# Kernel optimization log

Measured on AMD Instinct MI355X. Metric: run time of the kernel, lower is better.

Reference implementation:

```python
import jax, jax.numpy as jnp
import numpy as np

N = 320   # coalition size (number of prefix steps)
D = 512   # input_dim / attention weight_dim


def setup_inputs() -> dict:
    key = jax.random.key(0)
    ks = jax.random.split(key, 10)
    s = 1.0 / np.sqrt(D)  # torch Linear default init range
    u = lambda k, shape: jax.random.uniform(k, shape, jnp.float32, -s, s)
    return {
        "x": jax.random.normal(ks[0], (N, D), jnp.float32),
        "goal": jax.random.normal(ks[1], (D,), jnp.float32),
        "Wq": u(ks[2], (D, D)), "bq": u(ks[3], (D,)),
        "Wk": u(ks[4], (D, D)), "bk": u(ks[5], (D,)),
        "Wv": u(ks[6], (D, D)), "bv": u(ks[7], (D,)),
        # norm_col_init(std=0.1): small column-normalized weights; bias zero-filled
        "Wc": 0.01 * jax.random.normal(ks[8], (1, 2 * D), jnp.float32),
        "bc": jnp.zeros((1,), jnp.float32),
    }


def reference(x, goal, Wq, bq, Wk, bk, Wv, bv, Wc, bc):
    # x: [n, d] coalition features. goal is unused by the original forward.
    n, d = x.shape
    q = x @ Wq.T + bq  # [n, d]
    k = x @ Wk.T + bk
    v = x @ Wv.T + bv
    scores = (q @ k.T) / jnp.sqrt(jnp.asarray(d, x.dtype))  # [n, n]

    # Prefix lengths j = 1..n-1. For each j, attention over coalition[:j]:
    # softmax over keys < j (rows < j are the only valid queries), then the
    # AttentionLayer global feature = mean over query rows of attn @ v.
    j = jnp.arange(1, n)                          # [n-1]
    idx = jnp.arange(n)
    prefix_mask = idx[None, :] < j[:, None]       # [n-1, n], True for k < j
    neg = jnp.finfo(scores.dtype).min
    masked = jnp.where(prefix_mask[:, None, :], scores[None, :, :], neg)  # [n-1, n, n]
    att = jax.nn.softmax(masked, axis=-1)         # rows >= j are garbage, masked below
    # mean over valid query rows i < j, fused before multiplying by V:
    pooled = jnp.sum(att * prefix_mask[:, :, None], axis=1) / j[:, None].astype(x.dtype)  # [n-1, n]
    feats = pooled @ v                            # [n-1, d] global feature per prefix

    # j = 0 uses a zero feature vector
    features = jnp.concatenate([jnp.zeros((1, d), x.dtype), feats], axis=0)  # [n, d]
    cat = jnp.concatenate([features, x], axis=1)  # [n, 2d]
    vals = cat @ Wc.T + bc                        # [n, 1] critic outputs
    return jnp.sum(vals)[None]                    # scalar value, shape [1]
```

## Files before the change

kernel.cpp:

```cpp
#include <hip/hip_runtime.h>

#define NC 320
#define DIM 512

__global__ __launch_bounds__(256) void gemm_qk_part(
    const float* __restrict__ x,
    const float* __restrict__ Wq, const float* __restrict__ Wk,
    float* __restrict__ part)
{
  const int z = blockIdx.z;
  const float* __restrict__ W = (z & 8) ? Wk : Wq;
  const int kb = (z & 7) * 64;
  const int i0 = blockIdx.y * 64;
  const int c0 = blockIdx.x * 64;

  __shared__ __align__(16) float As[32][68];
  __shared__ __align__(16) float Bs[32][68];

  const int t  = threadIdx.x;
  const int sr = t >> 2;
  const int kc = (t & 3) << 3;
  const int ty = t >> 4;
  const int tx = t & 15;

  float acc[4][4] = {};

  const float* xp = x + (i0 + sr) * DIM + kc;
  const float* wp = W + (c0 + sr) * DIM + kc;

  for (int k0 = kb; k0 < kb + 64; k0 += 32) {
    const float4 xa = *(const float4*)(xp + k0);
    const float4 xb = *(const float4*)(xp + k0 + 4);
    const float4 wa = *(const float4*)(wp + k0);
    const float4 wb = *(const float4*)(wp + k0 + 4);
    __syncthreads();
    As[kc+0][sr]=xa.x; As[kc+1][sr]=xa.y; As[kc+2][sr]=xa.z; As[kc+3][sr]=xa.w;
    As[kc+4][sr]=xb.x; As[kc+5][sr]=xb.y; As[kc+6][sr]=xb.z; As[kc+7][sr]=xb.w;
    Bs[kc+0][sr]=wa.x; Bs[kc+1][sr]=wa.y; Bs[kc+2][sr]=wa.z; Bs[kc+3][sr]=wa.w;
    Bs[kc+4][sr]=wb.x; Bs[kc+5][sr]=wb.y; Bs[kc+6][sr]=wb.z; Bs[kc+7][sr]=wb.w;
    __syncthreads();
    #pragma unroll
    for (int kk = 0; kk < 32; ++kk) {
      const float4 a4 = *(const float4*)&As[kk][ty * 4];
      const float4 b4 = *(const float4*)&Bs[kk][tx * 4];
      const float a[4] = {a4.x, a4.y, a4.z, a4.w};
      const float b[4] = {b4.x, b4.y, b4.z, b4.w};
      #pragma unroll
      for (int i = 0; i < 4; ++i)
        #pragma unroll
        for (int j = 0; j < 4; ++j)
          acc[i][j] = fmaf(a[i], b[j], acc[i][j]);
    }
  }

  float* outp = part + (size_t)z * NC * DIM;
  #pragma unroll
  for (int i = 0; i < 4; ++i) {
    float4 o = {acc[i][0], acc[i][1], acc[i][2], acc[i][3]};
    *(float4*)&outp[(i0 + ty*4 + i) * DIM + c0 + tx*4] = o;
  }
}

__global__ __launch_bounds__(256) void reduce_qk(
    const float* __restrict__ part,
    const float* __restrict__ bq, const float* __restrict__ bk,
    float* __restrict__ q, float* __restrict__ k)
{
  const int mat = blockIdx.y;
  const int f   = blockIdx.x * 256 + threadIdx.x;
  const int row = f >> 7;
  const int col = (f & 127) * 4;
  const float* bias = mat ? bk : bq;
  float4 s = *(const float4*)&bias[col];
  const size_t off = (size_t)row * DIM + col;
  #pragma unroll
  for (int sp = 0; sp < 8; ++sp) {
    const float4 p = *(const float4*)&part[(size_t)(mat*8+sp) * NC * DIM + off];
    s.x += p.x; s.y += p.y; s.z += p.z; s.w += p.w;
  }
  float* out = mat ? k : q;
  *(float4*)&out[off] = s;
}

__global__ __launch_bounds__(256) void scores_part(
    const float* __restrict__ q, const float* __restrict__ k,
    float* __restrict__ part)
{
  const int z  = blockIdx.z;
  const int kb = z * 64;
  const int i0 = blockIdx.y * 64;
  const int j0 = blockIdx.x * 64;

  __shared__ __align__(16) float As[32][68];
  __shared__ __align__(16) float Bs[32][68];

  const int t  = threadIdx.x;
  const int sr = t >> 2;
  const int kc = (t & 3) << 3;
  const int ty = t >> 4;
  const int tx = t & 15;

  float acc[4][4] = {};

  const float* qp = q + (i0 + sr) * DIM + kc;
  const float* kp = k + (j0 + sr) * DIM + kc;

  for (int k0 = kb; k0 < kb + 64; k0 += 32) {
    const float4 qa = *(const float4*)(qp + k0);
    const float4 qb = *(const float4*)(qp + k0 + 4);
    const float4 ka = *(const float4*)(kp + k0);
    const float4 kb4= *(const float4*)(kp + k0 + 4);
    __syncthreads();
    As[kc+0][sr]=qa.x; As[kc+1][sr]=qa.y; As[kc+2][sr]=qa.z; As[kc+3][sr]=qa.w;
    As[kc+4][sr]=qb.x; As[kc+5][sr]=qb.y; As[kc+6][sr]=qb.z; As[kc+7][sr]=qb.w;
    Bs[kc+0][sr]=ka.x; Bs[kc+1][sr]=ka.y; Bs[kc+2][sr]=ka.z; Bs[kc+3][sr]=ka.w;
    Bs[kc+4][sr]=kb4.x;Bs[kc+5][sr]=kb4.y;Bs[kc+6][sr]=kb4.z;Bs[kc+7][sr]=kb4.w;
    __syncthreads();
    #pragma unroll
    for (int kk = 0; kk < 32; ++kk) {
      const float4 a4 = *(const float4*)&As[kk][ty * 4];
      const float4 b4 = *(const float4*)&Bs[kk][tx * 4];
      const float a[4] = {a4.x, a4.y, a4.z, a4.w};
      const float b[4] = {b4.x, b4.y, b4.z, b4.w};
      #pragma unroll
      for (int i = 0; i < 4; ++i)
        #pragma unroll
        for (int j = 0; j < 4; ++j)
          acc[i][j] = fmaf(a[i], b[j], acc[i][j]);
    }
  }

  float* outp = part + (size_t)z * NC * NC;
  #pragma unroll
  for (int i = 0; i < 4; ++i) {
    float4 o = {acc[i][0], acc[i][1], acc[i][2], acc[i][3]};
    *(float4*)&outp[(i0 + ty*4 + i) * NC + j0 + tx*4] = o;
  }
}

__global__ __launch_bounds__(256) void reduce_S(
    const float* __restrict__ part, float* __restrict__ S)
{
  const int f = blockIdx.x * 256 + threadIdx.x;
  const size_t off = (size_t)f * 4;
  float4 s = {0.f, 0.f, 0.f, 0.f};
  #pragma unroll
  for (int sp = 0; sp < 8; ++sp) {
    const float4 p = *(const float4*)&part[(size_t)sp * NC * NC + off];
    s.x += p.x; s.y += p.y; s.z += p.z; s.w += p.w;
  }
  const float scale = 0.044194173824159216f;
  s.x *= scale; s.y *= scale; s.z *= scale; s.w *= scale;
  *(float4*)&S[off] = s;
}

__global__ __launch_bounds__(256) void compute_h(
    const float* __restrict__ Wv, const float* __restrict__ Wc,
    float* __restrict__ h)
{
  const int e  = blockIdx.x * 256 + threadIdx.x;
  const int d0 = blockIdx.y * 32;
  float s = 0.f;
  #pragma unroll
  for (int d = 0; d < 32; ++d)
    s = fmaf(Wv[(d0 + d) * DIM + e], Wc[d0 + d], s);
  atomicAdd(&h[e], s);
}

__global__ __launch_bounds__(256) void row_ops(
    const float* __restrict__ S, float* __restrict__ P)
{
  const int i    = blockIdx.x;
  const int t    = threadIdx.x;
  const int lane = t & 63;
  const int wave = t >> 6;

  __shared__ float e[NC];
  __shared__ float Warr[NC];
  __shared__ float Csuf[NC + 1];
  __shared__ float wred[4];

  for (int kk = t; kk < NC; kk += 256) e[kk] = S[i * NC + kk];
  __syncthreads();

  float m = -1e30f;
  for (int kk = t; kk < NC; kk += 256) m = fmaxf(m, e[kk]);
  #pragma unroll
  for (int off = 32; off; off >>= 1) m = fmaxf(m, __shfl_down(m, off));
  if (lane == 0) wred[wave] = m;
  __syncthreads();
  m = fmaxf(fmaxf(wred[0], wred[1]), fmaxf(wred[2], wred[3]));

  for (int kk = t; kk < NC; kk += 256) e[kk] = __expf(e[kk] - m);
  __syncthreads();

  if (wave == 0) {
    float carry = 0.f;
    #pragma unroll
    for (int c = 0; c < 5; ++c) {
      const int idx = c * 64 + lane;
      float val = e[idx];
      #pragma unroll
      for (int off = 1; off < 64; off <<= 1) {
        const float nv = __shfl_up(val, off);
        if (lane >= off) val += nv;
      }
      const float incl = val + carry;
      const int j = idx + 1;
      if (j < NC) Warr[j] = (j > i) ? 1.f / ((float)j * incl) : 0.f;
      carry += __shfl(val, 63);
    }
    if (lane == 0) Warr[0] = 0.f;

    carry = 0.f;
    #pragma unroll
    for (int c = 4; c >= 0; --c) {
      const int idx = c * 64 + lane;
      float val = Warr[idx];
      #pragma unroll
      for (int off = 1; off < 64; off <<= 1) {
        const float nv = __shfl_down(val, off);
        if (lane + off < 64) val += nv;
      }
      Csuf[idx] = val + carry;
      carry += __shfl(val, 0);
    }
    if (lane == 0) Csuf[NC] = 0.f;
  }
  __syncthreads();

  for (int kk = t; kk < NC; kk += 256) {
    const int mm = (i > kk) ? i : kk;
    atomicAdd(&P[kk], e[kk] * Csuf[mm + 1]);
  }
}

__global__ __launch_bounds__(256) void finalize(
    const float* __restrict__ x, const float* __restrict__ P,
    const float* __restrict__ h, const float* __restrict__ Wc,
    const float* __restrict__ bc, const float* __restrict__ bv,
    float* __restrict__ out)
{
  const int kk   = blockIdx.x;
  const int t    = threadIdx.x;
  const int lane = t & 63;
  const int wave = t >> 6;

  __shared__ float tmp[4];
  __shared__ float tmp2[8];

  const float pk = P[kk];
  const float* xr = x + kk * DIM;
  float s = 0.f;
  for (int e = t; e < DIM; e += 256)
    s += xr[e] * fmaf(pk, h[e], Wc[DIM + e]);
  #pragma unroll
  for (int off = 32; off; off >>= 1) s += __shfl_down(s, off);
  if (lane == 0) tmp[wave] = s;

  if (kk == 0) {
    float ec = 0.f, ep = 0.f;
    for (int d = t; d < DIM; d += 256) ec += bv[d] * Wc[d];
    for (int mIdx = t; mIdx < NC; mIdx += 256) ep += P[mIdx];
    #pragma unroll
    for (int off = 32; off; off >>= 1) {
      ec += __shfl_down(ec, off);
      ep += __shfl_down(ep, off);
    }
    if (lane == 0) { tmp2[wave] = ec; tmp2[4 + wave] = ep; }
  }
  __syncthreads();

  if (t == 0) {
    float tot = tmp[0] + tmp[1] + tmp[2] + tmp[3];
    atomicAdd(out, tot);
    if (kk == 0) {
      const float c  = tmp2[0] + tmp2[1] + tmp2[2] + tmp2[3];
      const float sp = tmp2[4] + tmp2[5] + tmp2[6] + tmp2[7];
      atomicAdd(out, c * sp + (float)NC * bc[0]);
    }
  }
}

extern "C" void kernel_launch(void* const* d_in, const int* in_sizes, int n_in,
                              void* d_out, int out_size, void* d_ws, size_t ws_size,
                              hipStream_t stream) {
  const float* x  = (const float*)d_in[0];
  const float* Wq = (const float*)d_in[2];
  const float* bq = (const float*)d_in[3];
  const float* Wk = (const float*)d_in[4];
  const float* bk = (const float*)d_in[5];
  const float* Wv = (const float*)d_in[6];
  const float* bv = (const float*)d_in[7];
  const float* Wc = (const float*)d_in[8];
  const float* bc = (const float*)d_in[9];

  float* ws     = (float*)d_ws;
  float* q      = ws;
  float* k      = q + NC * DIM;
  float* S      = k + NC * DIM;
  float* P      = S + NC * NC;
  float* h      = P + NC;
  float* partQK = h + DIM;
  float* partS  = partQK + 16 * NC * DIM;
  float* out = (float*)d_out;

  hipMemsetAsync(P, 0, (NC + DIM) * sizeof(float), stream);
  hipMemsetAsync(out, 0, sizeof(float), stream);

  gemm_qk_part<<<dim3(8, 5, 16), 256, 0, stream>>>(x, Wq, Wk, partQK);
  reduce_qk<<<dim3(160, 2), 256, 0, stream>>>(partQK, bq, bk, q, k);
  compute_h<<<dim3(2, 16), 256, 0, stream>>>(Wv, Wc, h);
  scores_part<<<dim3(5, 5, 8), 256, 0, stream>>>(q, k, partS);
  reduce_S<<<100, 256, 0, stream>>>(partS, S);
  row_ops<<<NC, 256, 0, stream>>>(S, P);
  finalize<<<NC, 256, 0, stream>>>(x, P, h, Wc, bc, bv, out);
}
```

Before: 120.2 us.

## Fuse split-K reductions into consumers and precompute per-row critic projections

Removes reduce_qk and reduce_S by having the scores GEMM sum the Q/K split-K partials (plus biases) while loading tiles, and having the row softmax kernel sum the score partials on load. Replaces compute_h and finalize with one kernel that computes h = Wv^T Wc_feat and per-row u = x·h + c, accumulating the x·Wc_x term directly. row_ops then dots P with u in-block instead of atomically building P, cutting launch count from 7 to 4. The trade-off is redundant partial-sum reads: each scores tile re-reads 8 partials per Q/K element across 5 tile columns, and the hu kernel runs a serial 512-step loop per thread on only 20 blocks.

```diff
diff --git a/kernel.cpp b/kernel.cpp
--- a/kernel.cpp
+++ b/kernel.cpp
@@ -61,30 +61,73 @@
   }
 }
 
-__global__ __launch_bounds__(256) void reduce_qk(
+__global__ __launch_bounds__(256) void hu(
+    const float* __restrict__ x,  const float* __restrict__ Wv,
+    const float* __restrict__ bv, const float* __restrict__ Wc,
+    const float* __restrict__ bc,
+    float* __restrict__ u, float* __restrict__ out)
+{
+  const int t    = threadIdx.x;
+  const int lane = t & 63;
+  const int wave = t >> 6;
+
+  __shared__ __align__(16) float hsh[DIM];
+  __shared__ __align__(16) float wxs[DIM];
+  __shared__ float wsum[4];
+
+  float s0 = 0.f, s1 = 0.f;
+  #pragma unroll 8
+  for (int d = 0; d < DIM; ++d) {
+    const float wc = Wc[d];
+    s0 = fmaf(Wv[d * DIM + t],       wc, s0);
+    s1 = fmaf(Wv[d * DIM + t + 256], wc, s1);
+  }
+  hsh[t] = s0; hsh[t + 256] = s1;
+  wxs[t] = Wc[DIM + t]; wxs[t + 256] = Wc[DIM + t + 256];
+
+  float cp = bv[t] * Wc[t] + bv[t + 256] * Wc[t + 256];
+  #pragma unroll
+  for (int off = 32; off; off >>= 1) cp += __shfl_down(cp, off);
+  if (lane == 0) wsum[wave] = cp;
+  __syncthreads();
+  const float c = wsum[0] + wsum[1] + wsum[2] + wsum[3];
+
+  float wxp = 0.f;
+  const int rowbase = blockIdx.x * 16;
+  for (int rr = wave; rr < 16; rr += 4) {
+    const int r = rowbase + rr;
+    const float* xr = x + r * DIM;
+    float su = 0.f, sw = 0.f;
+    #pragma unroll
+    for (int mq = 0; mq < 2; ++mq) {
+      const int e0 = lane * 8 + mq * 4;
+      const float4 xv = *(const float4*)&xr[e0];
+      const float4 hv = *(const float4*)&hsh[e0];
+      const float4 wv = *(const float4*)&wxs[e0];
+      su += xv.x*hv.x + xv.y*hv.y + xv.z*hv.z + xv.w*hv.w;
+      sw += xv.x*wv.x + xv.y*wv.y + xv.z*wv.z + xv.w*wv.w;
+    }
+    #pragma unroll
+    for (int off = 32; off; off >>= 1) {
+      su += __shfl_down(su, off);
+      sw += __shfl_down(sw, off);
+    }
+    if (lane == 0) { u[r] = su + c; wxp += sw; }
+  }
+  __syncthreads();
+  if (lane == 0) wsum[wave] = wxp;
+  __syncthreads();
+  if (t == 0) {
+    float v = wsum[0] + wsum[1] + wsum[2] + wsum[3];
+    if (blockIdx.x == 0) v += (float)NC * bc[0];
+    atomicAdd(out, v);
+  }
+}
+
+__global__ __launch_bounds__(256) void scores_part2(
     const float* __restrict__ part,
     const float* __restrict__ bq, const float* __restrict__ bk,
-    float* __restrict__ q, float* __restrict__ k)
-{
-  const int mat = blockIdx.y;
-  const int f   = blockIdx.x * 256 + threadIdx.x;
-  const int row = f >> 7;
-  const int col = (f & 127) * 4;
-  const float* bias = mat ? bk : bq;
-  float4 s = *(const float4*)&bias[col];
-  const size_t off = (size_t)row * DIM + col;
-  #pragma unroll
-  for (int sp = 0; sp < 8; ++sp) {
-    const float4 p = *(const float4*)&part[(size_t)(mat*8+sp) * NC * DIM + off];
-    s.x += p.x; s.y += p.y; s.z += p.z; s.w += p.w;
-  }
-  float* out = mat ? k : q;
-  *(float4*)&out[off] = s;
-}
-
-__global__ __launch_bounds__(256) void scores_part(
-    const float* __restrict__ q, const float* __restrict__ k,
-    float* __restrict__ part)
+    float* __restrict__ partS)
 {
   const int z  = blockIdx.z;
   const int kb = z * 64;
@@ -102,19 +145,31 @@
 
   float acc[4][4] = {};
 
-  const float* qp = q + (i0 + sr) * DIM + kc;
-  const float* kp = k + (j0 + sr) * DIM + kc;
-
   for (int k0 = kb; k0 < kb + 64; k0 += 32) {
-    const float4 qa = *(const float4*)(qp + k0);
-    const float4 qb = *(const float4*)(qp + k0 + 4);
-    const float4 ka = *(const float4*)(kp + k0);
-    const float4 kb4= *(const float4*)(kp + k0 + 4);
+    float4 qa = *(const float4*)&bq[k0 + kc];
+    float4 qb = *(const float4*)&bq[k0 + kc + 4];
+    float4 ka = *(const float4*)&bk[k0 + kc];
+    float4 k2 = *(const float4*)&bk[k0 + kc + 4];
+    const size_t qoff = (size_t)(i0 + sr) * DIM + k0 + kc;
+    const size_t koff = (size_t)(j0 + sr) * DIM + k0 + kc;
+    #pragma unroll
+    for (int sp = 0; sp < 8; ++sp) {
+      const float* pq = part + (size_t)sp * (NC * DIM);
+      const float* pk = part + (size_t)(8 + sp) * (NC * DIM);
+      const float4 a0 = *(const float4*)(pq + qoff);
+      const float4 a1 = *(const float4*)(pq + qoff + 4);
+      const float4 b0 = *(const float4*)(pk + koff);
+      const float4 b1 = *(const float4*)(pk + koff + 4);
+      qa.x += a0.x; qa.y += a0.y; qa.z += a0.z; qa.w += a0.w;
+      qb.x += a1.x; qb.y += a1.y; qb.z += a1.z; qb.w += a1.w;
+      ka.x += b0.x; ka.y += b0.y; ka.z += b0.z; ka.w += b0.w;
+      k2.x += b1.x; k2.y += b1.y; k2.z += b1.z; k2.w += b1.w;
+    }
     __syncthreads();
     As[kc+0][sr]=qa.x; As[kc+1][sr]=qa.y; As[kc+2][sr]=qa.z; As[kc+3][sr]=qa.w;
     As[kc+4][sr]=qb.x; As[kc+5][sr]=qb.y; As[kc+6][sr]=qb.z; As[kc+7][sr]=qb.w;
     Bs[kc+0][sr]=ka.x; Bs[kc+1][sr]=ka.y; Bs[kc+2][sr]=ka.z; Bs[kc+3][sr]=ka.w;
-    Bs[kc+4][sr]=kb4.x;Bs[kc+5][sr]=kb4.y;Bs[kc+6][sr]=kb4.z;Bs[kc+7][sr]=kb4.w;
+    Bs[kc+4][sr]=k2.x; Bs[kc+5][sr]=k2.y; Bs[kc+6][sr]=k2.z; Bs[kc+7][sr]=k2.w;
     __syncthreads();
     #pragma unroll
     for (int kk = 0; kk < 32; ++kk) {
@@ -130,7 +185,7 @@
     }
   }
 
-  float* outp = part + (size_t)z * NC * NC;
+  float* outp = partS + (size_t)z * NC * NC;
   #pragma unroll
   for (int i = 0; i < 4; ++i) {
     float4 o = {acc[i][0], acc[i][1], acc[i][2], acc[i][3]};
@@ -138,37 +193,9 @@
   }
 }
 
-__global__ __launch_bounds__(256) void reduce_S(
-    const float* __restrict__ part, float* __restrict__ S)
-{
-  const int f = blockIdx.x * 256 + threadIdx.x;
-  const size_t off = (size_t)f * 4;
-  float4 s = {0.f, 0.f, 0.f, 0.f};
-  #pragma unroll
-  for (int sp = 0; sp < 8; ++sp) {
-    const float4 p = *(const float4*)&part[(size_t)sp * NC * NC + off];
-    s.x += p.x; s.y += p.y; s.z += p.z; s.w += p.w;
-  }
-  const float scale = 0.044194173824159216f;
-  s.x *= scale; s.y *= scale; s.z *= scale; s.w *= scale;
-  *(float4*)&S[off] = s;
-}
-
-__global__ __launch_bounds__(256) void compute_h(
-    const float* __restrict__ Wv, const float* __restrict__ Wc,
-    float* __restrict__ h)
-{
-  const int e  = blockIdx.x * 256 + threadIdx.x;
-  const int d0 = blockIdx.y * 32;
-  float s = 0.f;
-  #pragma unroll
-  for (int d = 0; d < 32; ++d)
-    s = fmaf(Wv[(d0 + d) * DIM + e], Wc[d0 + d], s);
-  atomicAdd(&h[e], s);
-}
-
-__global__ __launch_bounds__(256) void row_ops(
-    const float* __restrict__ S, float* __restrict__ P)
+__global__ __launch_bounds__(256) void row_ops2(
+    const float* __restrict__ partS, const float* __restrict__ u,
+    float* __restrict__ out)
 {
   const int i    = blockIdx.x;
   const int t    = threadIdx.x;
@@ -180,7 +207,14 @@
   __shared__ float Csuf[NC + 1];
   __shared__ float wred[4];
 
-  for (int kk = t; kk < NC; kk += 256) e[kk] = S[i * NC + kk];
+  const float scale = 0.044194173824159216f;
+  for (int kk = t; kk < NC; kk += 256) {
+    float s = 0.f;
+    #pragma unroll
+    for (int sp = 0; sp < 8; ++sp)
+      s += partS[(size_t)sp * NC * NC + i * NC + kk];
+    e[kk] = s * scale;
+  }
   __syncthreads();
 
   float m = -1e30f;
@@ -229,57 +263,18 @@
   }
   __syncthreads();
 
+  float acc = 0.f;
   for (int kk = t; kk < NC; kk += 256) {
     const int mm = (i > kk) ? i : kk;
-    atomicAdd(&P[kk], e[kk] * Csuf[mm + 1]);
-  }
-}
-
-__global__ __launch_bounds__(256) void finalize(
-    const float* __restrict__ x, const float* __restrict__ P,
-    const float* __restrict__ h, const float* __restrict__ Wc,
-    const float* __restrict__ bc, const float* __restrict__ bv,
-    float* __restrict__ out)
-{
-  const int kk   = blockIdx.x;
-  const int t    = threadIdx.x;
-  const int lane = t & 63;
-  const int wave = t >> 6;
-
-  __shared__ float tmp[4];
-  __shared__ float tmp2[8];
-
-  const float pk = P[kk];
-  const float* xr = x + kk * DIM;
-  float s = 0.f;
-  for (int e = t; e < DIM; e += 256)
-    s += xr[e] * fmaf(pk, h[e], Wc[DIM + e]);
-  #pragma unroll
-  for (int off = 32; off; off >>= 1) s += __shfl_down(s, off);
-  if (lane == 0) tmp[wave] = s;
-
-  if (kk == 0) {
-    float ec = 0.f, ep = 0.f;
-    for (int d = t; d < DIM; d += 256) ec += bv[d] * Wc[d];
-    for (int mIdx = t; mIdx < NC; mIdx += 256) ep += P[mIdx];
-    #pragma unroll
-    for (int off = 32; off; off >>= 1) {
-      ec += __shfl_down(ec, off);
-      ep += __shfl_down(ep, off);
-    }
-    if (lane == 0) { tmp2[wave] = ec; tmp2[4 + wave] = ep; }
-  }
-  __syncthreads();
-
-  if (t == 0) {
-    float tot = tmp[0] + tmp[1] + tmp[2] + tmp[3];
-    atomicAdd(out, tot);
-    if (kk == 0) {
-      const float c  = tmp2[0] + tmp2[1] + tmp2[2] + tmp2[3];
-      const float sp = tmp2[4] + tmp2[5] + tmp2[6] + tmp2[7];
-      atomicAdd(out, c * sp + (float)NC * bc[0]);
-    }
-  }
+    acc += e[kk] * Csuf[mm + 1] * u[kk];
+  }
+  #pragma unroll
+  for (int off = 32; off; off >>= 1) acc += __shfl_down(acc, off);
+  __syncthreads();
+  if (lane == 0) wred[wave] = acc;
+  __syncthreads();
+  if (t == 0)
+    atomicAdd(out, wred[0] + wred[1] + wred[2] + wred[3]);
 }
 
 extern "C" void kernel_launch(void* const* d_in, const int* in_sizes, int n_in,
@@ -296,23 +291,15 @@
   const float* bc = (const float*)d_in[9];
 
   float* ws     = (float*)d_ws;
-  float* q      = ws;
-  float* k      = q + NC * DIM;
-  float* S      = k + NC * DIM;
-  float* P      = S + NC * NC;
-  float* h      = P + NC;
-  float* partQK = h + DIM;
+  float* partQK = ws;
   float* partS  = partQK + 16 * NC * DIM;
-  float* out = (float*)d_out;
-
-  hipMemsetAsync(P, 0, (NC + DIM) * sizeof(float), stream);
+  float* u      = partS + 8 * NC * NC;
+  float* out    = (float*)d_out;
+
   hipMemsetAsync(out, 0, sizeof(float), stream);
 
   gemm_qk_part<<<dim3(8, 5, 16), 256, 0, stream>>>(x, Wq, Wk, partQK);
-  reduce_qk<<<dim3(160, 2), 256, 0, stream>>>(partQK, bq, bk, q, k);
-  compute_h<<<dim3(2, 16), 256, 0, stream>>>(Wv, Wc, h);
-  scores_part<<<dim3(5, 5, 8), 256, 0, stream>>>(q, k, partS);
-  reduce_S<<<100, 256, 0, stream>>>(partS, S);
-  row_ops<<<NC, 256, 0, stream>>>(S, P);
-  finalize<<<NC, 256, 0, stream>>>(x, P, h, Wc, bc, bv, out);
-}
+  hu<<<20, 256, 0, stream>>>(x, Wv, bv, Wc, bc, u, out);
+  scores_part2<<<dim3(5, 5, 8), 256, 0, stream>>>(partQK, bq, bk, partS);
+  row_ops2<<<NC, 256, 0, stream>>>(partS, u, out);
+}
```

After: 139.0 us. +15.6%, slower.
